# Kernel optimization log

Hardware: AMD Instinct MI355X
Metric: run time of the kernel (lower is better)

The kernel has to match this reference:

```python
import jax, jax.numpy as jnp
import numpy as np

B, S, D_IN, H, SD = 512, 1024, 64, 64, 4


def setup_inputs() -> dict:
    key = jax.random.key(0)
    ks = jax.random.split(key, 12)
    sc_in = 1.0 / np.sqrt(D_IN)
    sc_h = 1.0 / np.sqrt(H)
    sc_c = 1.0 / np.sqrt(SD + H)
    return {
        "x": jax.random.normal(ks[0], (B, S, D_IN), jnp.float32),
        "W1": jax.random.uniform(ks[1], (H, D_IN), jnp.float32, -sc_in, sc_in),
        "b1": jax.random.uniform(ks[2], (H,), jnp.float32, -sc_in, sc_in),
        "ln_g": jnp.ones((H,), jnp.float32),
        "ln_b": jnp.zeros((H,), jnp.float32),
        "Wi": jax.random.uniform(ks[3], (SD, H), jnp.float32, -sc_h, sc_h),
        "bi": jax.random.uniform(ks[4], (SD,), jnp.float32, -sc_h, sc_h),
        "Wc1": jax.random.uniform(ks[5], (H, SD + H), jnp.float32, -sc_c, sc_c),
        "bc1": jax.random.uniform(ks[6], (H,), jnp.float32, -sc_c, sc_c),
        "Wc2": jax.random.uniform(ks[7], (SD, H), jnp.float32, -sc_h, sc_h),
        "bc2": jax.random.uniform(ks[8], (SD,), jnp.float32, -sc_h, sc_h),
        "corr_scale": jnp.asarray(0.01, jnp.float32),
        "A_level": jnp.zeros((1,), jnp.float32),
        "A_trend": jnp.zeros((1,), jnp.float32),
        "A_gamma": jnp.zeros((1,), jnp.float32),
        "A_resid": jnp.zeros((1,), jnp.float32),
        "omega": jnp.zeros((1,), jnp.float32),
    }


def reference(x, W1, b1, ln_g, ln_b, Wi, bi, Wc1, bc1, Wc2, bc2,
              corr_scale, A_level, A_trend, A_gamma, A_resid, omega):
    # input_proj: Linear -> LayerNorm -> GELU (exact erf), dropout=0
    h = jnp.einsum('bsd,hd->bsh', x, W1) + b1
    mu = jnp.mean(h, axis=-1, keepdims=True)
    var = jnp.mean((h - mu) ** 2, axis=-1, keepdims=True)
    h = (h - mu) * jax.lax.rsqrt(var + 1e-5) * ln_g + ln_b
    h = jax.nn.gelu(h, approximate=False)  # [B,S,H]

    # structured A for state_dim == 4: diag(a_l, a_t, gamma*cos(w), a_r)
    a_l = jax.nn.sigmoid(A_level) * 0.15 + 0.85
    a_t = jax.nn.sigmoid(A_trend) * 0.25 + 0.7
    gamma = jax.nn.sigmoid(A_gamma) * 0.2 + 0.8
    a_r = jax.nn.sigmoid(A_resid) * 0.4
    A = jnp.diag(jnp.concatenate([a_l, a_t, gamma * jnp.cos(omega), a_r]))  # [4,4]

    # innovation applied to all steps at once (batched tiny GEMM)
    bx = jnp.einsum('bsh,kh->bsk', h, Wi) + bi  # [B,S,4]

    def step(s, inp):
        bx_t, h_t = inp  # [B,4], [B,H]
        s_lin = s @ A.T + bx_t
        corr_in = jnp.concatenate([s_lin, h_t], axis=-1)  # [B,4+H]
        c = jax.nn.gelu(corr_in @ Wc1.T + bc1, approximate=False) @ Wc2.T + bc2
        s_new = s_lin + corr_scale * jnp.tanh(c)
        return s_new, s_new

    s0 = jnp.zeros((x.shape[0], SD), x.dtype)
    _, outs = jax.lax.scan(step, s0, (bx.transpose(1, 0, 2), h.transpose(1, 0, 2)))
    return outs.transpose(1, 0, 2)  # [B,S,4] == return_all_states=True
```

## Files before the change

kernel.cpp:

```cpp
#include <hip/hip_runtime.h>
#include <hip/hip_bf16.h>

#define BB 512
#define SS 1024
#define DIN 64
#define HH 64
#define SD4 4
#define CH 64
#define LB 64

typedef __attribute__((ext_vector_type(8))) short s8v;
typedef __attribute__((ext_vector_type(4))) float f4v;

#define MFMA_BF16(a, b, c) __builtin_amdgcn_mfma_f32_16x16x32_bf16((a), (b), (c), 0, 0, 0)

template <int CTRL>
__device__ __forceinline__ float dppf(float v) {
    return __int_as_float(__builtin_amdgcn_mov_dpp(__float_as_int(v), CTRL, 0xF, 0xF, false));
}

__device__ __forceinline__ float rcp_fast(float x) {
    return __builtin_amdgcn_rcpf(x);
}
__device__ __forceinline__ unsigned int cvt_pk(float lo, float hi) {
    unsigned int r;
    asm("v_cvt_pk_bf16_f32 %0, %1, %2" : "=v"(r) : "v"(lo), "v"(hi));
    return r;
}
__device__ __forceinline__ float bf2f(unsigned short u) {
    return __uint_as_float(((unsigned int)u) << 16);
}
__device__ __forceinline__ float sigmoid_f(float x) {
    return 1.0f / (1.0f + __expf(-x));
}
__device__ __forceinline__ float tanh_fast(float x) {
    return fmaf(-2.0f, rcp_fast(__expf(2.0f * x) + 1.0f), 1.0f);
}
__device__ __forceinline__ float gelu_fast(float x) {
    float x2 = x * x;
    float z = x * fmaf(x2, -0.0713548162f, -1.5957691216f);
    return x * rcp_fast(1.0f + __expf(z));
}
__device__ __forceinline__ s8v cvt8(const float* __restrict__ p) {
    const float4* q4 = (const float4*)p;
    float4 a = q4[0], b = q4[1];
    union { s8v s; unsigned int u[4]; } r;
    r.u[0] = cvt_pk(a.x, a.y); r.u[1] = cvt_pk(a.z, a.w);
    r.u[2] = cvt_pk(b.x, b.y); r.u[3] = cvt_pk(b.z, b.w);
    return r.s;
}

__global__ __launch_bounds__(256)
void prep_mfma(const float* __restrict__ x,
               const float* __restrict__ W1, const float* __restrict__ b1,
               const float* __restrict__ ln_g, const float* __restrict__ ln_b,
               const float* __restrict__ Wi, const float* __restrict__ bi,
               const float* __restrict__ Wc1, const float* __restrict__ bc1,
               uint2* __restrict__ pre4, float* __restrict__ bx)
{
    __shared__ unsigned short hb[4][16 * 88];
    __shared__ unsigned short wcs[64 * 72];

    const int tid = threadIdx.x;
    const int wave = tid >> 6;
    const int lane = tid & 63;
    const int c = lane & 15;
    const int q = lane >> 4;

    const long tokW = ((long)blockIdx.x * 4 + wave) * 64;

    const float* xp = x + (tokW + c) * DIN + q * 8;
    float4 xf0 = *(const float4*)(xp + 0);
    float4 xf1 = *(const float4*)(xp + 4);
    float4 xf2 = *(const float4*)(xp + 32);
    float4 xf3 = *(const float4*)(xp + 36);
    xp += 16 * DIN;

    {
        const int row = tid >> 2, chn = tid & 3;
        const float4* s4 = (const float4*)(Wc1 + row * 68 + 4 + chn * 16);
        float4 f0 = s4[0], f1 = s4[1], f2 = s4[2], f3 = s4[3];
        uint2* dst = (uint2*)(wcs + row * 72 + chn * 16);
        dst[0] = make_uint2(cvt_pk(f0.x, f0.y), cvt_pk(f0.z, f0.w));
        dst[1] = make_uint2(cvt_pk(f1.x, f1.y), cvt_pk(f1.z, f1.w));
        dst[2] = make_uint2(cvt_pk(f2.x, f2.y), cvt_pk(f2.z, f2.w));
        dst[3] = make_uint2(cvt_pk(f3.x, f3.y), cvt_pk(f3.z, f3.w));
    }
    __syncthreads();

    s8v W1f[4][2], Wif[2];
#pragma unroll
    for (int n = 0; n < 4; ++n)
#pragma unroll
        for (int kh = 0; kh < 2; ++kh)
            W1f[n][kh] = cvt8(W1 + (4 * c + n) * DIN + q * 8 + kh * 32);
#pragma unroll
    for (int kh = 0; kh < 2; ++kh) {
        if (c < 4) {
            Wif[kh] = cvt8(Wi + c * HH + q * 8 + kh * 32);
        } else {
            s8v z;
#pragma unroll
            for (int e = 0; e < 8; ++e) z[e] = 0;
            Wif[kh] = z;
        }
    }

    float gln[4], bln[4], b1v[4], bc1v[4];
#pragma unroll
    for (int n = 0; n < 4; ++n) {
        const int j1 = 4 * c + n;
        const int j2 = c + 16 * n;
        gln[n] = ln_g[j1]; bln[n] = ln_b[j1]; b1v[n] = b1[j1];
        bc1v[n] = bc1[j2];
    }
    const float biv = (c < 4) ? bi[c] : 0.0f;

    unsigned short* Hb = hb[wave];
    uint2* pq = pre4 + ((tokW >> 2) + q) * 64 + c * 4;
    float* bq = bx + (tokW + q * 4) * SD4 + c;

    auto gemm1_ln = [&](s8v A0_, s8v A1_, uint2* hwo) {
        f4v acc[4];
#pragma unroll
        for (int n = 0; n < 4; ++n) {
            f4v z = { b1v[n], b1v[n], b1v[n], b1v[n] };
            z = MFMA_BF16(A0_, W1f[n][0], z);
            acc[n] = MFMA_BF16(A1_, W1f[n][1], z);
        }
        float sm[4], sq[4];
#pragma unroll
        for (int r = 0; r < 4; ++r) {
            sm[r] = acc[0][r] + acc[1][r] + acc[2][r] + acc[3][r];
            sq[r] = fmaf(acc[0][r], acc[0][r],
                    fmaf(acc[1][r], acc[1][r],
                    fmaf(acc[2][r], acc[2][r], acc[3][r] * acc[3][r])));
        }
#pragma unroll
        for (int r = 0; r < 4; ++r) { sm[r] += dppf<0x121>(sm[r]); sq[r] += dppf<0x121>(sq[r]); }
#pragma unroll
        for (int r = 0; r < 4; ++r) { sm[r] += dppf<0x122>(sm[r]); sq[r] += dppf<0x122>(sq[r]); }
#pragma unroll
        for (int r = 0; r < 4; ++r) { sm[r] += dppf<0x124>(sm[r]); sq[r] += dppf<0x124>(sq[r]); }
#pragma unroll
        for (int r = 0; r < 4; ++r) { sm[r] += dppf<0x128>(sm[r]); sq[r] += dppf<0x128>(sq[r]); }
#pragma unroll
        for (int r = 0; r < 4; ++r) {
            const float mu = sm[r] * (1.0f / HH);
            const float var = fmaf(-mu, mu, sq[r] * (1.0f / HH));
            const float rstd = rsqrtf(var + 1e-5f);
            float g0 = gelu_fast(fmaf((acc[0][r] - mu) * rstd, gln[0], bln[0]));
            float g1 = gelu_fast(fmaf((acc[1][r] - mu) * rstd, gln[1], bln[1]));
            float g2 = gelu_fast(fmaf((acc[2][r] - mu) * rstd, gln[2], bln[2]));
            float g3 = gelu_fast(fmaf((acc[3][r] - mu) * rstd, gln[3], bln[3]));
            hwo[r] = make_uint2(cvt_pk(g0, g1), cvt_pk(g2, g3));
        }
    };

    s8v A0, A1;
    {
        union { s8v s; unsigned int u[4]; } a;
        a.u[0] = cvt_pk(xf0.x, xf0.y); a.u[1] = cvt_pk(xf0.z, xf0.w);
        a.u[2] = cvt_pk(xf1.x, xf1.y); a.u[3] = cvt_pk(xf1.z, xf1.w);
        A0 = a.s;
        a.u[0] = cvt_pk(xf2.x, xf2.y); a.u[1] = cvt_pk(xf2.z, xf2.w);
        a.u[2] = cvt_pk(xf3.x, xf3.y); a.u[3] = cvt_pk(xf3.z, xf3.w);
        A1 = a.s;
    }
    xf0 = *(const float4*)(xp + 0);
    xf1 = *(const float4*)(xp + 4);
    xf2 = *(const float4*)(xp + 32);
    xf3 = *(const float4*)(xp + 36);
    xp += 16 * DIN;

    uint2 hw[4];
    gemm1_ln(A0, A1, hw);
#pragma unroll
    for (int r = 0; r < 4; ++r) *(uint2*)(Hb + (q * 4 + r) * 88 + 4 * c) = hw[r];

#pragma unroll 1
    for (int t = 0; t < 4; ++t) {
        s8v H0 = *(const s8v*)(Hb + c * 88 + q * 8);
        s8v H1 = *(const s8v*)(Hb + c * 88 + 32 + q * 8);

        uint2 hwn[4];
        if (t < 3) {
            union { s8v s; unsigned int u[4]; } a;
            a.u[0] = cvt_pk(xf0.x, xf0.y); a.u[1] = cvt_pk(xf0.z, xf0.w);
            a.u[2] = cvt_pk(xf1.x, xf1.y); a.u[3] = cvt_pk(xf1.z, xf1.w);
            s8v nA0 = a.s;
            a.u[0] = cvt_pk(xf2.x, xf2.y); a.u[1] = cvt_pk(xf2.z, xf2.w);
            a.u[2] = cvt_pk(xf3.x, xf3.y); a.u[3] = cvt_pk(xf3.z, xf3.w);
            s8v nA1 = a.s;
            if (t < 2) {
                xf0 = *(const float4*)(xp + 0);
                xf1 = *(const float4*)(xp + 4);
                xf2 = *(const float4*)(xp + 32);
                xf3 = *(const float4*)(xp + 36);
                xp += 16 * DIN;
            }
            gemm1_ln(nA0, nA1, hwn);
        }

        f4v p[4];
#pragma unroll
        for (int n = 0; n < 4; ++n) {
            const s8v Wf0 = *(const s8v*)(wcs + (c + 16 * n) * 72 + q * 8);
            const s8v Wf1 = *(const s8v*)(wcs + (c + 16 * n) * 72 + 32 + q * 8);
            f4v z = { bc1v[n], bc1v[n], bc1v[n], bc1v[n] };
            z = MFMA_BF16(H0, Wf0, z);
            p[n] = MFMA_BF16(H1, Wf1, z);
        }
        f4v bz = { biv, biv, biv, biv };
        bz = MFMA_BF16(H0, Wif[0], bz);
        bz = MFMA_BF16(H1, Wif[1], bz);

        if (c < 4) {
#pragma unroll
            for (int r = 0; r < 4; ++r) bq[r * SD4] = bz[r];
        }
        {
            uint2 u0 = make_uint2(cvt_pk(p[0][0], p[1][0]), cvt_pk(p[2][0], p[3][0]));
            uint2 u1 = make_uint2(cvt_pk(p[0][1], p[1][1]), cvt_pk(p[2][1], p[3][1]));
            uint2 u2 = make_uint2(cvt_pk(p[0][2], p[1][2]), cvt_pk(p[2][2], p[3][2]));
            uint2 u3 = make_uint2(cvt_pk(p[0][3], p[1][3]), cvt_pk(p[2][3], p[3][3]));
            *(uint4*)(pq)     = make_uint4(u0.x, u0.y, u1.x, u1.y);
            *(uint4*)(pq + 2) = make_uint4(u2.x, u2.y, u3.x, u3.y);
        }
        pq += 256; bq += 64;

        if (t < 3) {
#pragma unroll
            for (int r = 0; r < 4; ++r) *(uint2*)(Hb + (q * 4 + r) * 88 + 4 * c) = hwn[r];
        }
    }
}

__global__ __launch_bounds__(256)
void scan_chunk(const uint2* __restrict__ pre4, const float* __restrict__ bx,
                const float* __restrict__ Wc1, const float* __restrict__ Wc2,
                const float* __restrict__ bc2, const float* __restrict__ corr_scale,
                const float* __restrict__ A_level, const float* __restrict__ A_trend,
                const float* __restrict__ A_gamma, const float* __restrict__ A_resid,
                const float* __restrict__ omega, float* __restrict__ out)
{
    const int tid = threadIdx.x;
    const int g = tid >> 4;
    const int L = tid & 15;
    const int b = blockIdx.x;
    const int warm = (g == 0) ? 0 : LB;
    const int t0 = g * CH - warm;
    const int wend = warm + CH;
    const int myi = L >> 2;

    float w[4][4], v[4][4];
#pragma unroll
    for (int m = 0; m < 4; ++m) {
        const int j = L + 16 * m;
#pragma unroll
        for (int k = 0; k < 4; ++k) {
            w[m][k] = Wc1[j * 68 + k];
            v[k][m] = Wc2[k * HH + j];
        }
    }
    const float cs = corr_scale[0];
    const float a0 = sigmoid_f(A_level[0]) * 0.15f + 0.85f;
    const float a1 = sigmoid_f(A_trend[0]) * 0.25f + 0.70f;
    const float a2 = (sigmoid_f(A_gamma[0]) * 0.2f + 0.8f) * cosf(omega[0]);
    const float a3 = sigmoid_f(A_resid[0]) * 0.4f;
    const float csel = bc2[L & 3];
    const bool o1 = (L & 1) != 0;
    const bool o2 = (L & 2) != 0;

    const uint4* pp = (const uint4*)pre4 + (((long)b * SS + t0) >> 2) * 32 + L * 2;
    const float4* bp = (const float4*)bx + (long)b * SS + t0;
    float* op = out + ((long)b * SS + t0) * SD4;

    float s0 = 0.f, s1 = 0.f, s2 = 0.f, s3 = 0.f;

    auto step4 = [&](uint4 qa, uint4 qb, const float4* bv, int tt) {
        float oreg = 0.f;
#pragma unroll
        for (int i = 0; i < 4; ++i) {
            const unsigned int ux = (i == 0) ? qa.x : (i == 1) ? qa.z : (i == 2) ? qb.x : qb.z;
            const unsigned int uy = (i == 0) ? qa.y : (i == 1) ? qa.w : (i == 2) ? qb.y : qb.w;
            const float l0 = fmaf(a0, s0, bv[i].x);
            const float l1 = fmaf(a1, s1, bv[i].y);
            const float l2 = fmaf(a2, s2, bv[i].z);
            const float l3 = fmaf(a3, s3, bv[i].w);
            const float p0 = bf2f((unsigned short)(ux & 0xffffu));
            const float p1 = bf2f((unsigned short)(ux >> 16));
            const float p2 = bf2f((unsigned short)(uy & 0xffffu));
            const float p3 = bf2f((unsigned short)(uy >> 16));
            float gg[4];
            {
                float ua0 = fmaf(l0, w[0][0], p0), ub0 = fmaf(l2, w[0][2], l3 * w[0][3]);
                float ua1 = fmaf(l0, w[1][0], p1), ub1 = fmaf(l2, w[1][2], l3 * w[1][3]);
                float ua2 = fmaf(l0, w[2][0], p2), ub2 = fmaf(l2, w[2][2], l3 * w[2][3]);
                float ua3 = fmaf(l0, w[3][0], p3), ub3 = fmaf(l2, w[3][2], l3 * w[3][3]);
                gg[0] = gelu_fast(fmaf(l1, w[0][1], ua0) + ub0);
                gg[1] = gelu_fast(fmaf(l1, w[1][1], ua1) + ub1);
                gg[2] = gelu_fast(fmaf(l1, w[2][1], ua2) + ub2);
                gg[3] = gelu_fast(fmaf(l1, w[3][1], ua3) + ub3);
            }
            const float P0 = fmaf(gg[0], v[0][0], gg[1] * v[0][1]) + fmaf(gg[2], v[0][2], gg[3] * v[0][3]);
            const float P1 = fmaf(gg[0], v[1][0], gg[1] * v[1][1]) + fmaf(gg[2], v[1][2], gg[3] * v[1][3]);
            const float P2 = fmaf(gg[0], v[2][0], gg[1] * v[2][1]) + fmaf(gg[2], v[2][2], gg[3] * v[2][3]);
            const float P3 = fmaf(gg[0], v[3][0], gg[1] * v[3][1]) + fmaf(gg[2], v[3][2], gg[3] * v[3][3]);
            const float k0 = o1 ? P1 : P0, s0s = o1 ? P0 : P1;
            const float k1 = o1 ? P3 : P2, s1s = o1 ? P2 : P3;
            const float Af = k0 + dppf<0xB1>(s0s);
            const float Bf = k1 + dppf<0xB1>(s1s);
            const float kk = o2 ? Bf : Af, ss = o2 ? Af : Bf;
            float T = kk + dppf<0x4E>(ss);
            T += dppf<0x124>(T);
            T += dppf<0x128>(T);
            const float th = tanh_fast(T + csel);
            const float lsel = o2 ? (o1 ? l3 : l2) : (o1 ? l1 : l0);
            const float sval = fmaf(cs, th, lsel);
            s0 = dppf<0x00>(sval);
            s1 = dppf<0x55>(sval);
            s2 = dppf<0xAA>(sval);
            s3 = dppf<0xFF>(sval);
            if (myi == i) oreg = sval;
        }
        if (tt >= warm && tt < wend) op[tt * SD4 + L] = oreg;
    };

    uint4 qa0 = pp[0],  qb0 = pp[1];
    uint4 qa1 = pp[32], qb1 = pp[33];
    float4 bA[4], bB[4];
#pragma unroll
    for (int i = 0; i < 4; ++i) { bA[i] = bp[i]; bB[i] = bp[4 + i]; }

#pragma unroll 1
    for (int tt = 0; tt < 2 * CH; tt += 8) {
        const int pf0 = (tt + 8  < 2 * CH) ? (tt + 8)  : (2 * CH - 8);
        const int pf1 = (tt + 12 < 2 * CH) ? (tt + 12) : (2 * CH - 8);
        const uint4* p0 = pp + (pf0 >> 2) * 32;
        const uint4* p1 = pp + (pf1 >> 2) * 32;
        uint4 nqa0 = p0[0], nqb0 = p0[1];
        uint4 nqa1 = p1[0], nqb1 = p1[1];
        float4 nbA[4], nbB[4];
#pragma unroll
        for (int i = 0; i < 4; ++i) { nbA[i] = bp[pf0 + i]; nbB[i] = bp[pf1 + i]; }

        step4(qa0, qb0, bA, tt);
        step4(qa1, qb1, bB, tt + 4);

        qa0 = nqa0; qb0 = nqb0; qa1 = nqa1; qb1 = nqb1;
#pragma unroll
        for (int i = 0; i < 4; ++i) { bA[i] = nbA[i]; bB[i] = nbB[i]; }
    }
}

extern "C" void kernel_launch(void* const* d_in, const int* in_sizes, int n_in,
                              void* d_out, int out_size, void* d_ws, size_t ws_size,
                              hipStream_t stream) {
    (void)in_sizes; (void)n_in; (void)out_size; (void)ws_size;
    const float* x    = (const float*)d_in[0];
    const float* W1   = (const float*)d_in[1];
    const float* b1   = (const float*)d_in[2];
    const float* ln_g = (const float*)d_in[3];
    const float* ln_b = (const float*)d_in[4];
    const float* Wi   = (const float*)d_in[5];
    const float* bi   = (const float*)d_in[6];
    const float* Wc1  = (const float*)d_in[7];
    const float* bc1  = (const float*)d_in[8];
    const float* Wc2  = (const float*)d_in[9];
    const float* bc2  = (const float*)d_in[10];
    const float* corr = (const float*)d_in[11];
    const float* Al   = (const float*)d_in[12];
    const float* At   = (const float*)d_in[13];
    const float* Ag   = (const float*)d_in[14];
    const float* Ar   = (const float*)d_in[15];
    const float* om   = (const float*)d_in[16];

    uint2* pre4 = (uint2*)d_ws;
    float* bx = (float*)((char*)d_ws + (size_t)BB * SS * 16 * sizeof(uint2));
    float* out = (float*)d_out;

    prep_mfma<<<dim3(2048), dim3(256), 0, stream>>>(
        x, W1, b1, ln_g, ln_b, Wi, bi, Wc1, bc1, pre4, bx);
    scan_chunk<<<dim3(BB), dim3(256), 0, stream>>>(
        pre4, bx, Wc1, Wc2, bc2, corr, Al, At, Ag, Ar, om, out);
}
```

Baseline: 299.5 us.

## Interleave two independent scan chunks per thread group to hide dependency latency

```diff
diff --git a/kernel.cpp b/kernel.cpp
--- a/kernel.cpp
+++ b/kernel.cpp
@@ -236,7 +236,7 @@
     }
 }
 
-__global__ __launch_bounds__(256)
+__global__ __launch_bounds__(128)
 void scan_chunk(const uint2* __restrict__ pre4, const float* __restrict__ bx,
                 const float* __restrict__ Wc1, const float* __restrict__ Wc2,
                 const float* __restrict__ bc2, const float* __restrict__ corr_scale,
@@ -248,10 +248,10 @@
     const int g = tid >> 4;
     const int L = tid & 15;
     const int b = blockIdx.x;
-    const int warm = (g == 0) ? 0 : LB;
-    const int t0 = g * CH - warm;
-    const int wend = warm + CH;
-    const int myi = L >> 2;
+    const int cA = g, cB = g + 8;
+    const int warmA = (cA == 0) ? 0 : LB;
+    const int t0A = cA * CH - warmA;
+    const int t0B = cB * CH - LB;
 
     float w[4][4], v[4][4];
 #pragma unroll
@@ -271,23 +271,32 @@
     const float csel = bc2[L & 3];
     const bool o1 = (L & 1) != 0;
     const bool o2 = (L & 2) != 0;
-
-    const uint4* pp = (const uint4*)pre4 + (((long)b * SS + t0) >> 2) * 32 + L * 2;
-    const float4* bp = (const float4*)bx + (long)b * SS + t0;
-    float* op = out + ((long)b * SS + t0) * SD4;
-
-    float s0 = 0.f, s1 = 0.f, s2 = 0.f, s3 = 0.f;
-
-    auto step4 = [&](uint4 qa, uint4 qb, const float4* bv, int tt) {
+    const int myi = L >> 2;
+
+    const uint4* ppA = (const uint4*)pre4 + (((long)b * SS + t0A) >> 2) * 32 + L * 2;
+    const uint4* ppB = (const uint4*)pre4 + (((long)b * SS + t0B) >> 2) * 32 + L * 2;
+    const float4* bpA = (const float4*)bx + (long)b * SS + t0A;
+    const float4* bpB = (const float4*)bx + (long)b * SS + t0B;
+    float* opA = out + ((long)b * SS + t0A) * SD4;
+    float* opB = out + ((long)b * SS + t0B) * SD4;
+
+    float As0 = 0.f, As1 = 0.f, As2 = 0.f, As3 = 0.f;
+    float Bs0 = 0.f, Bs1 = 0.f, Bs2 = 0.f, Bs3 = 0.f;
+
+    auto core4 = [&](const uint4& qa, const uint4& qb,
+                     const float4& bv0, const float4& bv1,
+                     const float4& bv2, const float4& bv3,
+                     float& s0, float& s1, float& s2, float& s3) -> float {
         float oreg = 0.f;
 #pragma unroll
         for (int i = 0; i < 4; ++i) {
             const unsigned int ux = (i == 0) ? qa.x : (i == 1) ? qa.z : (i == 2) ? qb.x : qb.z;
             const unsigned int uy = (i == 0) ? qa.y : (i == 1) ? qa.w : (i == 2) ? qb.y : qb.w;
-            const float l0 = fmaf(a0, s0, bv[i].x);
-            const float l1 = fmaf(a1, s1, bv[i].y);
-            const float l2 = fmaf(a2, s2, bv[i].z);
-            const float l3 = fmaf(a3, s3, bv[i].w);
+            const float4 bv = (i == 0) ? bv0 : (i == 1) ? bv1 : (i == 2) ? bv2 : bv3;
+            const float l0 = fmaf(a0, s0, bv.x);
+            const float l1 = fmaf(a1, s1, bv.y);
+            const float l2 = fmaf(a2, s2, bv.z);
+            const float l3 = fmaf(a3, s3, bv.w);
             const float p0 = bf2f((unsigned short)(ux & 0xffffu));
             const float p1 = bf2f((unsigned short)(ux >> 16));
             const float p2 = bf2f((unsigned short)(uy & 0xffffu));
@@ -324,33 +333,43 @@
             s3 = dppf<0xFF>(sval);
             if (myi == i) oreg = sval;
         }
-        if (tt >= warm && tt < wend) op[tt * SD4 + L] = oreg;
+        return oreg;
     };
 
-    uint4 qa0 = pp[0],  qb0 = pp[1];
-    uint4 qa1 = pp[32], qb1 = pp[33];
-    float4 bA[4], bB[4];
-#pragma unroll
-    for (int i = 0; i < 4; ++i) { bA[i] = bp[i]; bB[i] = bp[4 + i]; }
+    auto refill = [&](uint4& qa, uint4& qb, float4& bv0, float4& bv1,
+                      float4& bv2, float4& bv3,
+                      const uint4* pp, const float4* bp, int pf) {
+        const uint4* p = pp + (pf >> 2) * 32;
+        qa = p[0]; qb = p[1];
+        bv0 = bp[pf]; bv1 = bp[pf + 1]; bv2 = bp[pf + 2]; bv3 = bp[pf + 3];
+    };
+
+    uint4 EAqa, EAqb, OAqa, OAqb, EBqa, EBqb, OBqa, OBqb;
+    float4 EAb0, EAb1, EAb2, EAb3, OAb0, OAb1, OAb2, OAb3;
+    float4 EBb0, EBb1, EBb2, EBb3, OBb0, OBb1, OBb2, OBb3;
+    refill(EAqa, EAqb, EAb0, EAb1, EAb2, EAb3, ppA, bpA, 0);
+    refill(EBqa, EBqb, EBb0, EBb1, EBb2, EBb3, ppB, bpB, 0);
+    refill(OAqa, OAqb, OAb0, OAb1, OAb2, OAb3, ppA, bpA, 4);
+    refill(OBqa, OBqb, OBb0, OBb1, OBb2, OBb3, ppB, bpB, 4);
 
 #pragma unroll 1
-    for (int tt = 0; tt < 2 * CH; tt += 8) {
-        const int pf0 = (tt + 8  < 2 * CH) ? (tt + 8)  : (2 * CH - 8);
-        const int pf1 = (tt + 12 < 2 * CH) ? (tt + 12) : (2 * CH - 8);
-        const uint4* p0 = pp + (pf0 >> 2) * 32;
-        const uint4* p1 = pp + (pf1 >> 2) * 32;
-        uint4 nqa0 = p0[0], nqb0 = p0[1];
-        uint4 nqa1 = p1[0], nqb1 = p1[1];
-        float4 nbA[4], nbB[4];
-#pragma unroll
-        for (int i = 0; i < 4; ++i) { nbA[i] = bp[pf0 + i]; nbB[i] = bp[pf1 + i]; }
-
-        step4(qa0, qb0, bA, tt);
-        step4(qa1, qb1, bB, tt + 4);
-
-        qa0 = nqa0; qb0 = nqb0; qa1 = nqa1; qb1 = nqb1;
-#pragma unroll
-        for (int i = 0; i < 4; ++i) { bA[i] = nbA[i]; bB[i] = nbB[i]; }
+    for (int it = 0; it < 2 * CH; it += 8) {
+        const int pfE = (it + 8  < 2 * CH) ? (it + 8)  : (2 * CH - 4);
+        const int pfO = (it + 12 < 2 * CH) ? (it + 12) : (2 * CH - 4);
+
+        const float oAe = core4(EAqa, EAqb, EAb0, EAb1, EAb2, EAb3, As0, As1, As2, As3);
+        const float oBe = core4(EBqa, EBqb, EBb0, EBb1, EBb2, EBb3, Bs0, Bs1, Bs2, Bs3);
+        if ((unsigned)(it - warmA) < (unsigned)CH) opA[it * SD4 + L] = oAe;
+        if (it >= LB)                              opB[it * SD4 + L] = oBe;
+        refill(EAqa, EAqb, EAb0, EAb1, EAb2, EAb3, ppA, bpA, pfE);
+        refill(EBqa, EBqb, EBb0, EBb1, EBb2, EBb3, ppB, bpB, pfE);
+
+        const float oAo = core4(OAqa, OAqb, OAb0, OAb1, OAb2, OAb3, As0, As1, As2, As3);
+        const float oBo = core4(OBqa, OBqb, OBb0, OBb1, OBb2, OBb3, Bs0, Bs1, Bs2, Bs3);
+        if ((unsigned)(it + 4 - warmA) < (unsigned)CH) opA[(it + 4) * SD4 + L] = oAo;
+        if (it + 4 >= LB)                              opB[(it + 4) * SD4 + L] = oBo;
+        refill(OAqa, OAqb, OAb0, OAb1, OAb2, OAb3, ppA, bpA, pfO);
+        refill(OBqa, OBqb, OBb0, OBb1, OBb2, OBb3, ppB, bpB, pfO);
     }
 }
 
@@ -382,6 +401,6 @@
 
     prep_mfma<<<dim3(2048), dim3(256), 0, stream>>>(
         x, W1, b1, ln_g, ln_b, Wi, bi, Wc1, bc1, pre4, bx);
-    scan_chunk<<<dim3(BB), dim3(256), 0, stream>>>(
+    scan_chunk<<<dim3(BB), dim3(128), 0, stream>>>(
         pre4, bx, Wc1, Wc2, bc2, corr, Al, At, Ag, Ar, om, out);
 }
```

New measurement: 351.3 us. 17.3% more time.
